# Kernel tuning notes

Hardware: AMD Instinct MI355X
Metric: run time of the kernel (lower is better)

The kernel has to match this reference:

```python
import jax, jax.numpy as jnp
import numpy as np

T, K, H, E, I = 128, 8, 2048, 64, 768


def setup_inputs() -> dict:
    key = jax.random.key(0)
    k1, k2, k3, k4, k5, k6 = jax.random.split(key, 6)
    return {
        "hidden_states": jax.random.normal(k1, (T, H), dtype=jnp.float32),
        "top_k_index": jax.random.randint(k2, (T, K), 0, E, dtype=jnp.int64),
        "top_k_weights": jax.random.uniform(k3, (T, K), dtype=jnp.float32),
        "w_gate": jax.random.normal(k4, (E, H, I), dtype=jnp.float32) * 0.02,
        "w_up": jax.random.normal(k5, (E, H, I), dtype=jnp.float32) * 0.02,
        "w_down": jax.random.normal(k6, (E, I, H), dtype=jnp.float32) * 0.02,
    }


def reference(hidden_states, top_k_index, top_k_weights, w_gate, w_up, w_down):
    # Per-token routed SwiGLU experts (Qwen3.5 MoE expert block):
    #   out_t = sum_k w_tk * down_{e_tk}( silu(gate_{e_tk}(x_t)) * up_{e_tk}(x_t) )
    h = hidden_states.astype(jnp.float32)  # [T, H]
    gate = jnp.einsum("td,edh->eth", h, w_gate)  # [E, T, I]
    up = jnp.einsum("td,edh->eth", h, w_up)      # [E, T, I]
    act = jax.nn.silu(gate) * up                 # [E, T, I]
    out_all = jnp.einsum("eti,eih->eth", act, w_down)  # [E, T, H]
    t_idx = jnp.arange(h.shape[0])
    sel = out_all[top_k_index, t_idx[:, None]]   # [T, K, H]
    out = jnp.sum(sel * top_k_weights[..., None], axis=1)  # [T, H]
    return out
```

## Files before the change

kernel.cpp:

```cpp
#include <hip/hip_runtime.h>
#include <stdint.h>

constexpr int Tn = 128;
constexpr int Kn = 8;
constexpr int Hn = 2048;
constexpr int En = 64;
constexpr int In = 768;
constexpr int NP = Tn * Kn;
constexpr int NTI = In / 128;
constexpr int DS = 4;
constexpr int DSL = Hn / DS;
constexpr int DSB = 2;
constexpr int ISL = In / DSB;

__global__ void route_kernel(const int* __restrict__ idx32,
                             int* __restrict__ offsets,
                             int* __restrict__ entries) {
  __shared__ int s_cnt[En];
  __shared__ int s_cur[En];
  __shared__ int s_odd_or;
  const int tid = threadIdx.x;
  if (tid == 0) s_odd_or = 0;
  if (tid < En) s_cnt[tid] = 0;
  __syncthreads();
  if (tid < NP / 2) {
    if (idx32[2 * tid + 1] != 0) atomicOr(&s_odd_or, 1);
  }
  __syncthreads();
  const bool is64 = (s_odd_or == 0);
  const int e = is64 ? idx32[2 * tid] : idx32[tid];
  atomicAdd(&s_cnt[e], 1);
  __syncthreads();
  if (tid == 0) {
    int acc = 0;
    for (int i = 0; i < En; ++i) { s_cur[i] = acc; offsets[i] = acc; acc += s_cnt[i]; }
    offsets[En] = acc;
  }
  __syncthreads();
  const int pos = atomicAdd(&s_cur[e], 1);
  entries[pos] = tid;
}

__global__ __launch_bounds__(256, 2) void gateup_clone(
    const float* __restrict__ hs, const float* __restrict__ wg,
    const float* __restrict__ wu, const int* __restrict__ offsets,
    const int* __restrict__ entries, float* __restrict__ gu) {
  const int b = blockIdx.x;
  const int ds = b & (DS - 1);
  const int tile = (b >> 2) % NTI;
  const int em = (b >> 2) / NTI;
  const int e = em & 63;
  const int m = em >> 6;
  const int beg = offsets[e];
  const int cnt = offsets[e + 1] - beg;
  if (cnt == 0) return;

  const int wave = threadIdx.x >> 6;
  const int lane = threadIdx.x & 63;
  const int dbeg = ds * DSL;
  const int col = tile * 128 + lane * 2;

  __shared__ float s_h[32][64];
  __shared__ int s_tok[32];

  const float* W = m ? wu : wg;
  const float* wp = W + (size_t)e * Hn * In + col;
  float* gup = gu + (size_t)m * NP * In;

  for (int chunk = 0; chunk < cnt; chunk += 32) {
    __syncthreads();
    if (threadIdx.x < 32) {
      const int r = threadIdx.x;
      s_tok[r] = entries[beg + chunk + min(r, cnt - chunk - 1)] >> 3;
    }
    __syncthreads();

    float2 acc[8];
#pragma unroll
    for (int j = 0; j < 8; ++j) acc[j] = make_float2(0.f, 0.f);

    for (int d0 = dbeg; d0 < dbeg + DSL; d0 += 64) {
      {
        const int r = threadIdx.x >> 3;
        const int g = (threadIdx.x & 7) * 8;
        const float* src = hs + (size_t)s_tok[r] * Hn + d0 + g;
        const float4 a = *reinterpret_cast<const float4*>(src);
        const float4 b4 = *reinterpret_cast<const float4*>(src + 4);
        *reinterpret_cast<float4*>(&s_h[r][g]) = a;
        *reinterpret_cast<float4*>(&s_h[r][g + 4]) = b4;
      }
      __syncthreads();
      const float* wdd = wp + (size_t)d0 * In;
#pragma unroll 2
      for (int dg = 0; dg < 64; dg += 4) {
        float2 wv[4];
#pragma unroll
        for (int q = 0; q < 4; ++q)
          wv[q] = *reinterpret_cast<const float2*>(wdd + (size_t)(dg + q) * In);
#pragma unroll
        for (int j = 0; j < 8; ++j) {
          const float4 hv = *reinterpret_cast<const float4*>(&s_h[wave * 8 + j][dg]);
          const float hvv[4] = {hv.x, hv.y, hv.z, hv.w};
#pragma unroll
          for (int q = 0; q < 4; ++q) {
            acc[j].x = fmaf(hvv[q], wv[q].x, acc[j].x);
            acc[j].y = fmaf(hvv[q], wv[q].y, acc[j].y);
          }
        }
      }
      __syncthreads();
    }

#pragma unroll
    for (int j = 0; j < 8; ++j) {
      const int r = wave * 8 + j;
      if (chunk + r < cnt) {
        const size_t ap = (size_t)(beg + chunk + r) * In + col;
        atomicAdd(&gup[ap], acc[j].x);
        atomicAdd(&gup[ap + 1], acc[j].y);
      }
    }
  }
}

__global__ void silu_kernel(float* __restrict__ gu) {
  const int i = blockIdx.x * blockDim.x + threadIdx.x;
  float4* g4 = reinterpret_cast<float4*>(gu);
  const float4* u4 = reinterpret_cast<const float4*>(gu + (size_t)NP * In);
  float4 g = g4[i];
  const float4 u = u4[i];
  g.x = g.x / (1.f + __expf(-g.x)) * u.x;
  g.y = g.y / (1.f + __expf(-g.y)) * u.y;
  g.z = g.z / (1.f + __expf(-g.z)) * u.z;
  g.w = g.w / (1.f + __expf(-g.w)) * u.w;
  g4[i] = g;
}

__global__ __launch_bounds__(256, 2) void down_split(
    const float* __restrict__ act, const float* __restrict__ wd,
    const float* __restrict__ tkw, const int* __restrict__ offsets,
    const int* __restrict__ entries, float* __restrict__ out) {
  const int b = blockIdx.x;
  const int isl = b & (DSB - 1);
  const int tile = (b >> 1) & 15;
  const int e = b >> 5;
  const int beg = offsets[e];
  const int cnt = offsets[e + 1] - beg;
  if (cnt == 0) return;

  const int wave = threadIdx.x >> 6;
  const int lane = threadIdx.x & 63;
  const int col = tile * 128 + lane * 2;
  const int ibeg = isl * ISL;

  __shared__ float s_a[32][64];
  __shared__ int s_tok[32];
  __shared__ int s_arow[32];
  __shared__ float s_w[32];

  const float* wdp = wd + (size_t)e * In * Hn + col;

  for (int chunk = 0; chunk < cnt; chunk += 32) {
    __syncthreads();
    if (threadIdx.x < 32) {
      const int r = threadIdx.x;
      const int rr = min(r, cnt - chunk - 1);
      const int p = entries[beg + chunk + rr];
      s_tok[r] = p >> 3;
      s_w[r] = tkw[p];
      s_arow[r] = beg + chunk + rr;
    }
    __syncthreads();

    float2 acc[8];
#pragma unroll
    for (int j = 0; j < 8; ++j) acc[j] = make_float2(0.f, 0.f);

    for (int i0 = ibeg; i0 < ibeg + ISL; i0 += 64) {
      {
        const int r = threadIdx.x >> 3;
        const int g = (threadIdx.x & 7) * 8;
        const float* src = act + (size_t)s_arow[r] * In + i0 + g;
        const float4 a = *reinterpret_cast<const float4*>(src);
        const float4 b4 = *reinterpret_cast<const float4*>(src + 4);
        *reinterpret_cast<float4*>(&s_a[r][g]) = a;
        *reinterpret_cast<float4*>(&s_a[r][g + 4]) = b4;
      }
      __syncthreads();
      const float* wdi = wdp + (size_t)i0 * Hn;
#pragma unroll 2
      for (int ig = 0; ig < 64; ig += 4) {
        float2 wdv[4];
#pragma unroll
        for (int q = 0; q < 4; ++q)
          wdv[q] = *reinterpret_cast<const float2*>(wdi + (size_t)(ig + q) * Hn);
#pragma unroll
        for (int j = 0; j < 8; ++j) {
          const float4 av = *reinterpret_cast<const float4*>(&s_a[wave * 8 + j][ig]);
          const float avv[4] = {av.x, av.y, av.z, av.w};
#pragma unroll
          for (int q = 0; q < 4; ++q) {
            acc[j].x = fmaf(avv[q], wdv[q].x, acc[j].x);
            acc[j].y = fmaf(avv[q], wdv[q].y, acc[j].y);
          }
        }
      }
      __syncthreads();
    }

#pragma unroll
    for (int j = 0; j < 8; ++j) {
      const int r = wave * 8 + j;
      if (chunk + r < cnt) {
        const float w = s_w[r];
        float* op = out + (size_t)s_tok[r] * Hn + col;
        atomicAdd(op, w * acc[j].x);
        atomicAdd(op + 1, w * acc[j].y);
      }
    }
  }
}

extern "C" void kernel_launch(void* const* d_in, const int* in_sizes, int n_in,
                              void* d_out, int out_size, void* d_ws, size_t ws_size,
                              hipStream_t stream) {
  const float* hs  = (const float*)d_in[0];
  const int*   idx = (const int*)d_in[1];
  const float* tkw = (const float*)d_in[2];
  const float* wg  = (const float*)d_in[3];
  const float* wu  = (const float*)d_in[4];
  const float* wd  = (const float*)d_in[5];
  float* out = (float*)d_out;

  char* ws = (char*)d_ws;
  int* offsets = (int*)ws;
  int* entries = (int*)(ws + 512);
  float* gu    = (float*)(ws + 8192);
  const size_t gu_bytes = (size_t)2 * NP * In * sizeof(float);

  route_kernel<<<1, NP, 0, stream>>>(idx, offsets, entries);
  hipMemsetAsync(d_out, 0, (size_t)Tn * Hn * sizeof(float), stream);
  hipMemsetAsync(gu, 0, gu_bytes, stream);
  gateup_clone<<<2 * En * NTI * DS, 256, 0, stream>>>(hs, wg, wu, offsets, entries, gu);
  silu_kernel<<<NP * In / 4 / 256, 256, 0, stream>>>(gu);
  down_split<<<En * 16 * DSB, 256, 0, stream>>>(gu, wd, tkw, offsets, entries, out);
}
```

Baseline: 457.3 us.

## Widen gate/up column tiles, add row-count specialization, drop down-proj I split

The gate/up kernel now has each lane compute four output columns using float4 weight loads, which halves the column tiles per expert. A templated body picks 4 or 8 rows per wave depending on how many tokens are in the chunk, so small chunks skip wasted FMAs. The down projection no longer splits the I dimension across two blocks, which halves its atomic traffic but also halves block count and parallelism. Wider tiles raise register pressure and give fewer blocks for latency hiding.

```diff
diff --git a/kernel.cpp b/kernel.cpp
--- a/kernel.cpp
+++ b/kernel.cpp
@@ -7,11 +7,9 @@
 constexpr int En = 64;
 constexpr int In = 768;
 constexpr int NP = Tn * Kn;
-constexpr int NTI = In / 128;
+constexpr int CT = 3;
 constexpr int DS = 4;
 constexpr int DSL = Hn / DS;
-constexpr int DSB = 2;
-constexpr int ISL = In / DSB;
 
 __global__ void route_kernel(const int* __restrict__ idx32,
                              int* __restrict__ offsets,
@@ -41,24 +39,90 @@
   entries[pos] = tid;
 }
 
-__global__ __launch_bounds__(256, 2) void gateup_clone(
+template <int RPW>
+__device__ __forceinline__ void guw_body(
+    const float* __restrict__ hs, const float* __restrict__ wp,
+    const int* __restrict__ s_tok, float (*__restrict__ s_h)[64],
+    int t, int wave, int dbeg, int cntc, size_t ap0,
+    float* __restrict__ gup) {
+  float4 acc[RPW];
+#pragma unroll
+  for (int j = 0; j < RPW; ++j) acc[j] = make_float4(0.f, 0.f, 0.f, 0.f);
+
+  for (int d0 = dbeg; d0 < dbeg + DSL; d0 += 64) {
+    {
+      const int r = t >> 3;
+      const int g = (t & 7) * 8;
+      const float* src = hs + (size_t)s_tok[r] * Hn + d0 + g;
+      const float4 a = *reinterpret_cast<const float4*>(src);
+      const float4 b4 = *reinterpret_cast<const float4*>(src + 4);
+      *reinterpret_cast<float4*>(&s_h[r][g]) = a;
+      *reinterpret_cast<float4*>(&s_h[r][g + 4]) = b4;
+    }
+    __syncthreads();
+    const float* wdd = wp + (size_t)d0 * In;
+#pragma unroll 2
+    for (int dg = 0; dg < 64; dg += 4) {
+      float4 wv[4];
+#pragma unroll
+      for (int q = 0; q < 4; ++q)
+        wv[q] = *reinterpret_cast<const float4*>(wdd + (size_t)(dg + q) * In);
+#pragma unroll
+      for (int j = 0; j < RPW; ++j) {
+        const float4 hv = *reinterpret_cast<const float4*>(&s_h[wave * RPW + j][dg]);
+        acc[j].x = fmaf(hv.x, wv[0].x, acc[j].x);
+        acc[j].y = fmaf(hv.x, wv[0].y, acc[j].y);
+        acc[j].z = fmaf(hv.x, wv[0].z, acc[j].z);
+        acc[j].w = fmaf(hv.x, wv[0].w, acc[j].w);
+        acc[j].x = fmaf(hv.y, wv[1].x, acc[j].x);
+        acc[j].y = fmaf(hv.y, wv[1].y, acc[j].y);
+        acc[j].z = fmaf(hv.y, wv[1].z, acc[j].z);
+        acc[j].w = fmaf(hv.y, wv[1].w, acc[j].w);
+        acc[j].x = fmaf(hv.z, wv[2].x, acc[j].x);
+        acc[j].y = fmaf(hv.z, wv[2].y, acc[j].y);
+        acc[j].z = fmaf(hv.z, wv[2].z, acc[j].z);
+        acc[j].w = fmaf(hv.z, wv[2].w, acc[j].w);
+        acc[j].x = fmaf(hv.w, wv[3].x, acc[j].x);
+        acc[j].y = fmaf(hv.w, wv[3].y, acc[j].y);
+        acc[j].z = fmaf(hv.w, wv[3].z, acc[j].z);
+        acc[j].w = fmaf(hv.w, wv[3].w, acc[j].w);
+      }
+    }
+    __syncthreads();
+  }
+
+#pragma unroll
+  for (int j = 0; j < RPW; ++j) {
+    const int row = wave * RPW + j;
+    if (row < cntc) {
+      const size_t ap = ap0 + (size_t)row * In;
+      atomicAdd(&gup[ap], acc[j].x);
+      atomicAdd(&gup[ap + 1], acc[j].y);
+      atomicAdd(&gup[ap + 2], acc[j].z);
+      atomicAdd(&gup[ap + 3], acc[j].w);
+    }
+  }
+}
+
+__global__ __launch_bounds__(256, 2) void gateup_wide(
     const float* __restrict__ hs, const float* __restrict__ wg,
     const float* __restrict__ wu, const int* __restrict__ offsets,
     const int* __restrict__ entries, float* __restrict__ gu) {
   const int b = blockIdx.x;
   const int ds = b & (DS - 1);
-  const int tile = (b >> 2) % NTI;
-  const int em = (b >> 2) / NTI;
+  const int tile = (b >> 2) % CT;
+  const int em = (b >> 2) / CT;
   const int e = em & 63;
   const int m = em >> 6;
   const int beg = offsets[e];
   const int cnt = offsets[e + 1] - beg;
   if (cnt == 0) return;
 
-  const int wave = threadIdx.x >> 6;
-  const int lane = threadIdx.x & 63;
+  const int t = threadIdx.x;
+  const int wave = t >> 6;
+  const int lane = t & 63;
   const int dbeg = ds * DSL;
-  const int col = tile * 128 + lane * 2;
+  const int col = tile * 256 + lane * 4;
 
   __shared__ float s_h[32][64];
   __shared__ int s_tok[32];
@@ -68,58 +132,17 @@
   float* gup = gu + (size_t)m * NP * In;
 
   for (int chunk = 0; chunk < cnt; chunk += 32) {
-    __syncthreads();
-    if (threadIdx.x < 32) {
-      const int r = threadIdx.x;
-      s_tok[r] = entries[beg + chunk + min(r, cnt - chunk - 1)] >> 3;
-    }
-    __syncthreads();
-
-    float2 acc[8];
-#pragma unroll
-    for (int j = 0; j < 8; ++j) acc[j] = make_float2(0.f, 0.f);
-
-    for (int d0 = dbeg; d0 < dbeg + DSL; d0 += 64) {
-      {
-        const int r = threadIdx.x >> 3;
-        const int g = (threadIdx.x & 7) * 8;
-        const float* src = hs + (size_t)s_tok[r] * Hn + d0 + g;
-        const float4 a = *reinterpret_cast<const float4*>(src);
-        const float4 b4 = *reinterpret_cast<const float4*>(src + 4);
-        *reinterpret_cast<float4*>(&s_h[r][g]) = a;
-        *reinterpret_cast<float4*>(&s_h[r][g + 4]) = b4;
-      }
-      __syncthreads();
-      const float* wdd = wp + (size_t)d0 * In;
-#pragma unroll 2
-      for (int dg = 0; dg < 64; dg += 4) {
-        float2 wv[4];
-#pragma unroll
-        for (int q = 0; q < 4; ++q)
-          wv[q] = *reinterpret_cast<const float2*>(wdd + (size_t)(dg + q) * In);
-#pragma unroll
-        for (int j = 0; j < 8; ++j) {
-          const float4 hv = *reinterpret_cast<const float4*>(&s_h[wave * 8 + j][dg]);
-          const float hvv[4] = {hv.x, hv.y, hv.z, hv.w};
-#pragma unroll
-          for (int q = 0; q < 4; ++q) {
-            acc[j].x = fmaf(hvv[q], wv[q].x, acc[j].x);
-            acc[j].y = fmaf(hvv[q], wv[q].y, acc[j].y);
-          }
-        }
-      }
-      __syncthreads();
-    }
-
-#pragma unroll
-    for (int j = 0; j < 8; ++j) {
-      const int r = wave * 8 + j;
-      if (chunk + r < cnt) {
-        const size_t ap = (size_t)(beg + chunk + r) * In + col;
-        atomicAdd(&gup[ap], acc[j].x);
-        atomicAdd(&gup[ap + 1], acc[j].y);
-      }
-    }
+    const int cntc = min(cnt - chunk, 32);
+
+    __syncthreads();
+    if (t < 32) s_tok[t] = entries[beg + chunk + min(t, cntc - 1)] >> 3;
+    __syncthreads();
+
+    const size_t ap0 = (size_t)(beg + chunk) * In + col;
+    if (cntc <= 16)
+      guw_body<4>(hs, wp, s_tok, s_h, t, wave, dbeg, cntc, ap0, gup);
+    else
+      guw_body<8>(hs, wp, s_tok, s_h, t, wave, dbeg, cntc, ap0, gup);
   }
 }
 
@@ -136,14 +159,12 @@
   g4[i] = g;
 }
 
-__global__ __launch_bounds__(256, 2) void down_split(
+__global__ __launch_bounds__(256, 2) void down_kernel(
     const float* __restrict__ act, const float* __restrict__ wd,
     const float* __restrict__ tkw, const int* __restrict__ offsets,
     const int* __restrict__ entries, float* __restrict__ out) {
-  const int b = blockIdx.x;
-  const int isl = b & (DSB - 1);
-  const int tile = (b >> 1) & 15;
-  const int e = b >> 5;
+  const int e = blockIdx.x >> 4;
+  const int tile = blockIdx.x & 15;
   const int beg = offsets[e];
   const int cnt = offsets[e + 1] - beg;
   if (cnt == 0) return;
@@ -151,7 +172,6 @@
   const int wave = threadIdx.x >> 6;
   const int lane = threadIdx.x & 63;
   const int col = tile * 128 + lane * 2;
-  const int ibeg = isl * ISL;
 
   __shared__ float s_a[32][64];
   __shared__ int s_tok[32];
@@ -176,7 +196,7 @@
 #pragma unroll
     for (int j = 0; j < 8; ++j) acc[j] = make_float2(0.f, 0.f);
 
-    for (int i0 = ibeg; i0 < ibeg + ISL; i0 += 64) {
+    for (int i0 = 0; i0 < In; i0 += 64) {
       {
         const int r = threadIdx.x >> 3;
         const int g = (threadIdx.x & 7) * 8;
@@ -241,7 +261,7 @@
   route_kernel<<<1, NP, 0, stream>>>(idx, offsets, entries);
   hipMemsetAsync(d_out, 0, (size_t)Tn * Hn * sizeof(float), stream);
   hipMemsetAsync(gu, 0, gu_bytes, stream);
-  gateup_clone<<<2 * En * NTI * DS, 256, 0, stream>>>(hs, wg, wu, offsets, entries, gu);
+  gateup_wide<<<2 * En * CT * DS, 256, 0, stream>>>(hs, wg, wu, offsets, entries, gu);
   silu_kernel<<<NP * In / 4 / 256, 256, 0, stream>>>(gu);
-  down_split<<<En * 16 * DSB, 256, 0, stream>>>(gu, wd, tkw, offsets, entries, out);
-}
+  down_kernel<<<En * (Hn / 128), 256, 0, stream>>>(gu, wd, tkw, offsets, entries, out);
+}
```

After: 425.8 us. 1.07x faster.
